# Kernel optimization log

Hardware: AMD Instinct MI355X
Metric: run time of the kernel (lower is better)

The kernel has to match this reference:

```python
import jax, jax.numpy as jnp
import numpy as np

NUM_EMBEDDINGS = 1024
EMBEDDING_DIM = 64
COMMITMENT_COST = 0.25


def setup_inputs() -> dict:
    key = jax.random.key(0)
    k1, k2 = jax.random.split(key)
    inputs = jax.random.normal(k1, (16, EMBEDDING_DIM, 64, 64), dtype=jnp.float32)
    # nn.Embedding weight init: uniform(-1/K, 1/K)
    emb = jax.random.uniform(
        k2, (NUM_EMBEDDINGS, EMBEDDING_DIM), dtype=jnp.float32,
        minval=-1.0 / NUM_EMBEDDINGS, maxval=1.0 / NUM_EMBEDDINGS)
    return {"inputs": inputs, "emb": emb}


def reference(inputs, emb):
    # NCHW -> NHWC
    x = jnp.transpose(inputs, (0, 2, 3, 1))  # [B,H,W,D]
    B, H, W, D = x.shape
    K = emb.shape[0]
    flat = x.reshape(-1, D)  # [N,D]

    # squared L2 distances to every codebook entry: [N,K]
    distances = (jnp.sum(flat * flat, axis=1, keepdims=True)
                 + jnp.sum(emb * emb, axis=1)
                 - 2.0 * jnp.matmul(flat, emb.T))
    idx = jnp.argmin(distances, axis=1)  # [N]
    indices = idx.reshape(B, H, W)[:, None]  # [B,1,H,W]

    # gather == one-hot @ emb, but without the dense matmul
    quantized = emb[idx].reshape(B, H, W, D)

    e_latent_loss = jnp.mean((jax.lax.stop_gradient(quantized) - x) ** 2)
    q_latent_loss = jnp.mean((quantized - jax.lax.stop_gradient(x)) ** 2)
    loss = q_latent_loss + COMMITMENT_COST * e_latent_loss

    # straight-through estimator
    quantized_st = x + jax.lax.stop_gradient(quantized - x)

    # one-hot encodings are part of the module's return contract
    encodings = jax.nn.one_hot(idx, K, dtype=jnp.float32)  # [N,K]
    avg_probs = jnp.mean(encodings, axis=0)
    perplexity = jnp.exp(-jnp.sum(avg_probs * jnp.log(avg_probs + 1e-10)))

    quantized_out = jnp.transpose(quantized_st, (0, 3, 1, 2))  # back to NCHW
    return (loss, quantized_out, perplexity, encodings, indices)
```

## Files before the change

kernel.cpp:

```cpp
#include <hip/hip_runtime.h>

#define NPIX    65536
#define D       64
#define KCODES  1024
#define PIXB    64
#define BLOCK   512
#define XPAD    68
#define CAP     64
#define GFAC    0.036f

#define QUANT_OFF 1
#define PERP_OFF  4194305
#define ENC_OFF   4194306u
#define IDX_OFF   71303170u

typedef float f32x4 __attribute__((ext_vector_type(4)));
typedef short bf16x8 __attribute__((ext_vector_type(8)));

__device__ __forceinline__ unsigned short f2bf(float f) {
    unsigned u = __float_as_uint(f);
    return (unsigned short)((u + 0x7fffu + ((u >> 16) & 1u)) >> 16);
}
__device__ __forceinline__ bf16x8 pack8(const float* p) {
    bf16x8 v;
    v[0] = (short)f2bf(p[0]); v[1] = (short)f2bf(p[1]);
    v[2] = (short)f2bf(p[2]); v[3] = (short)f2bf(p[3]);
    v[4] = (short)f2bf(p[4]); v[5] = (short)f2bf(p[5]);
    v[6] = (short)f2bf(p[6]); v[7] = (short)f2bf(p[7]);
    return v;
}

__global__ __launch_bounds__(256) void vq_init(const float* __restrict__ emb,
                                               double* __restrict__ loss_sum,
                                               int* __restrict__ counts,
                                               float* __restrict__ se) {
    int t = blockIdx.x * 256 + threadIdx.x;
    if (t == 0) *loss_sum = 0.0;
    if (t < KCODES) {
        counts[t] = 0;
        const float* e = emb + (size_t)t * D;
        float r[8];
        #pragma unroll
        for (int j = 0; j < 8; ++j) r[j] = __fmul_rn(e[j], e[j]);
        #pragma unroll
        for (int i = 8; i < D; i += 8)
            #pragma unroll
            for (int j = 0; j < 8; ++j)
                r[j] = __fadd_rn(r[j], __fmul_rn(e[i + j], e[i + j]));
        float X = __fadd_rn(__fadd_rn(r[0], r[1]), __fadd_rn(r[2], r[3]));
        float Y = __fadd_rn(__fadd_rn(r[4], r[5]), __fadd_rn(r[6], r[7]));
        se[t] = __fadd_rn(X, Y);
    }
}

__global__ __launch_bounds__(512) void vq_main(const float* __restrict__ in,
                                               const float* __restrict__ emb,
                                               const float* __restrict__ se,
                                               float* __restrict__ out,
                                               double* __restrict__ loss_sum,
                                               int* __restrict__ counts) {
    __shared__ float xs[PIXB][XPAD];
    __shared__ float sls[KCODES];
    __shared__ float wmin[8][PIXB];
    __shared__ float gate[PIXB];
    __shared__ float sxs[PIXB];
    __shared__ float smx[PIXB];
    __shared__ float semaxsq;
    __shared__ int   cnt[PIXB];
    __shared__ unsigned short list[PIXB][CAP];
    __shared__ int   skfin[PIXB];

    const int tid  = threadIdx.x;
    const int lane = tid & 63;
    const int wid  = tid >> 6;
    const int n0   = blockIdx.x * PIXB;
    const int b    = n0 >> 12;
    const int s0   = n0 & 4095;

    {
        const float* base = in + ((size_t)b << 18) + s0;
        #pragma unroll
        for (int i = 0; i < 8; ++i) {
            int d = wid + (i << 3);
            xs[lane][d] = base[((size_t)d << 12) + lane];
        }
        sls[tid] = se[tid];
        sls[tid + 512] = se[tid + 512];
    }
    __syncthreads();

    if (tid < PIXB) {
        float r[8];
        #pragma unroll
        for (int j = 0; j < 8; ++j) {
            float v = xs[tid][j];
            r[j] = __fmul_rn(v, v);
        }
        #pragma unroll
        for (int i = 8; i < D; i += 8)
            #pragma unroll
            for (int j = 0; j < 8; ++j) {
                float v = xs[tid][i + j];
                r[j] = __fadd_rn(r[j], __fmul_rn(v, v));
            }
        float X = __fadd_rn(__fadd_rn(r[0], r[1]), __fadd_rn(r[2], r[3]));
        float Y = __fadd_rn(__fadd_rn(r[4], r[5]), __fadd_rn(r[6], r[7]));
        sxs[tid] = __fadd_rn(X, Y);
        float mx = sls[tid << 4];
        #pragma unroll
        for (int j = 1; j < 16; ++j) mx = fmaxf(mx, sls[(tid << 4) + j]);
        smx[tid] = mx;
    }

    const int wbase = wid * 128;
    const int arow  = lane & 15;
    const int kgrp  = (lane >> 4) << 3;
    const int rbase = (lane >> 4) << 2;

    float mreg[4][4];
    #pragma unroll
    for (int pt = 0; pt < 4; ++pt)
        #pragma unroll
        for (int r = 0; r < 4; ++r) mreg[pt][r] = 3.0e38f;

    #pragma unroll
    for (int s = 0; s < 2; ++s) {
        const int cbase = wbase + s * 64;
        f32x4 acc[4][4];
        #pragma unroll
        for (int pt = 0; pt < 4; ++pt)
            #pragma unroll
            for (int kt = 0; kt < 4; ++kt) acc[pt][kt] = (f32x4){0.f, 0.f, 0.f, 0.f};
        #pragma unroll
        for (int ks = 0; ks < 2; ++ks) {
            bf16x8 af[4];
            #pragma unroll
            for (int pt = 0; pt < 4; ++pt)
                af[pt] = pack8(&xs[pt * 16 + arow][ks * 32 + kgrp]);
            #pragma unroll
            for (int kt = 0; kt < 4; ++kt) {
                int code = cbase + kt * 16 + arow;
                bf16x8 bf_ = pack8(emb + ((size_t)code << 6) + ks * 32 + kgrp);
                #pragma unroll
                for (int pt = 0; pt < 4; ++pt)
                    acc[pt][kt] = __builtin_amdgcn_mfma_f32_16x16x32_bf16(
                        af[pt], bf_, acc[pt][kt], 0, 0, 0);
            }
        }
        #pragma unroll
        for (int pt = 0; pt < 4; ++pt)
            #pragma unroll
            for (int kt = 0; kt < 4; ++kt) {
                int code = cbase + kt * 16 + arow;
                #pragma unroll
                for (int r = 0; r < 4; ++r) {
                    float sv = __fsub_rn(sls[code], __fmul_rn(2.0f, acc[pt][kt][r]));
                    mreg[pt][r] = fminf(mreg[pt][r], sv);
                }
            }
    }
    #pragma unroll
    for (int m = 1; m < 16; m <<= 1)
        #pragma unroll
        for (int pt = 0; pt < 4; ++pt)
            #pragma unroll
            for (int r = 0; r < 4; ++r)
                mreg[pt][r] = fminf(mreg[pt][r], __shfl_xor(mreg[pt][r], m));
    if (arow == 0) {
        #pragma unroll
        for (int pt = 0; pt < 4; ++pt)
            #pragma unroll
            for (int r = 0; r < 4; ++r)
                wmin[wid][pt * 16 + rbase + r] = mreg[pt][r];
    }
    __syncthreads();

    if (tid == 0) {
        float mx = smx[0];
        #pragma unroll
        for (int j = 1; j < PIXB; ++j) mx = fmaxf(mx, smx[j]);
        semaxsq = mx;
    }
    __syncthreads();

    if (tid < PIXB) {
        float gm = wmin[0][tid];
        #pragma unroll
        for (int w = 1; w < 8; ++w) gm = fminf(gm, wmin[w][tid]);
        gate[tid] = gm + GFAC * sqrtf(sxs[tid] * semaxsq);
        cnt[tid] = 0;
    }
    __syncthreads();

    #pragma unroll
    for (int s = 0; s < 2; ++s) {
        const int cbase = wbase + s * 64;
        f32x4 acc[4][4];
        #pragma unroll
        for (int pt = 0; pt < 4; ++pt)
            #pragma unroll
            for (int kt = 0; kt < 4; ++kt) acc[pt][kt] = (f32x4){0.f, 0.f, 0.f, 0.f};
        #pragma unroll
        for (int ks = 0; ks < 2; ++ks) {
            bf16x8 af[4];
            #pragma unroll
            for (int pt = 0; pt < 4; ++pt)
                af[pt] = pack8(&xs[pt * 16 + arow][ks * 32 + kgrp]);
            #pragma unroll
            for (int kt = 0; kt < 4; ++kt) {
                int code = cbase + kt * 16 + arow;
                bf16x8 bf_ = pack8(emb + ((size_t)code << 6) + ks * 32 + kgrp);
                #pragma unroll
                for (int pt = 0; pt < 4; ++pt)
                    acc[pt][kt] = __builtin_amdgcn_mfma_f32_16x16x32_bf16(
                        af[pt], bf_, acc[pt][kt], 0, 0, 0);
            }
        }
        #pragma unroll
        for (int pt = 0; pt < 4; ++pt)
            #pragma unroll
            for (int kt = 0; kt < 4; ++kt) {
                int code = cbase + kt * 16 + arow;
                #pragma unroll
                for (int r = 0; r < 4; ++r) {
                    float sv = __fsub_rn(sls[code], __fmul_rn(2.0f, acc[pt][kt][r]));
                    int px = pt * 16 + rbase + r;
                    if (sv <= gate[px]) {
                        int slot = atomicAdd(&cnt[px], 1);
                        if (slot < CAP) list[px][slot] = (unsigned short)code;
                    }
                }
            }
    }
    __syncthreads();

    {
        const int px = tid >> 3, c0 = tid & 7;
        const int cn = cnt[px];
        float bv = 3.0e38f;
        int   bk = 0x7fffffff;
        if (cn > CAP) {
            for (int k = c0; k < KCODES; k += 8) {
                const float* er = emb + ((size_t)k << 6);
                float m = 0.f;
                #pragma unroll
                for (int d = 0; d < D; ++d) m = fmaf(xs[px][d], er[d], m);
                float sv = __fsub_rn(__fadd_rn(sxs[px], sls[k]), __fmul_rn(2.0f, m));
                if (sv < bv || (sv == bv && k < bk)) { bv = sv; bk = k; }
            }
        } else {
            for (int i = c0; i < cn; i += 8) {
                int k = list[px][i];
                const float* er = emb + ((size_t)k << 6);
                float m = 0.f;
                #pragma unroll
                for (int d = 0; d < D; ++d) m = fmaf(xs[px][d], er[d], m);
                float sv = __fsub_rn(__fadd_rn(sxs[px], sls[k]), __fmul_rn(2.0f, m));
                if (sv < bv || (sv == bv && k < bk)) { bv = sv; bk = k; }
            }
        }
        #pragma unroll
        for (int m = 4; m; m >>= 1) {
            float ov = __shfl_xor(bv, m);
            int   ok = __shfl_xor(bk, m);
            if (ov < bv || (ov == bv && ok < bk)) { bv = ov; bk = ok; }
        }
        if (c0 == 0) {
            skfin[px] = bk;
            atomicAdd(&counts[bk], 1);
            out[IDX_OFF + (unsigned)(n0 + px)] = (float)bk;
        }
    }
    __syncthreads();

    if (tid < PIXB) {
        int bk2 = skfin[tid];
        const float* eq = emb + ((size_t)bk2 << 6);
        float* qout = out + QUANT_OFF + ((size_t)b << 18) + s0 + tid;
        float mse = 0.f;
        #pragma unroll
        for (int d = 0; d < D; ++d) {
            float q = eq[d];
            qout[(size_t)d << 12] = q;
            float df = q - xs[tid][d];
            mse = fmaf(df, df, mse);
        }
        #pragma unroll
        for (int off = 32; off; off >>= 1) mse += __shfl_down(mse, off);
        if (tid == 0) atomicAdd(loss_sum, (double)mse);
    }

    float4* dst4 = (float4*)(out + ENC_OFF + (size_t)n0 * KCODES + 2);
    for (int i = tid; i < 16383; i += BLOCK) {
        int flat = (i << 2) + 2;
        int r0 = flat >> 10;
        int r1 = (flat + 3) >> 10;
        int k0 = skfin[r0];
        int k1 = skfin[r1];
        int c  = flat & 1023;
        float4 v;
        v.x = (c == k0) ? 1.f : 0.f;
        v.y = (c + 1 == k0) ? 1.f : 0.f;
        v.z = (((flat + 2) & 1023) == k1) ? 1.f : 0.f;
        v.w = (((flat + 3) & 1023) == k1) ? 1.f : 0.f;
        dst4[i] = v;
    }
    if (tid == 0) {
        float2* dh = (float2*)(out + ENC_OFF + (size_t)n0 * KCODES);
        int kh = skfin[0];
        float2 h2; h2.x = (kh == 0) ? 1.f : 0.f; h2.y = (kh == 1) ? 1.f : 0.f;
        *dh = h2;
        float2* dt = (float2*)(out + ENC_OFF + (size_t)n0 * KCODES + 65534);
        int kt = skfin[63];
        float2 t2; t2.x = (kt == 1022) ? 1.f : 0.f; t2.y = (kt == 1023) ? 1.f : 0.f;
        *dt = t2;
    }
}

__global__ __launch_bounds__(256) void vq_fin(const double* __restrict__ loss_sum,
                                              const int* __restrict__ counts,
                                              float* __restrict__ out) {
    __shared__ double red[256];
    int t = threadIdx.x;
    double ent = 0.0;
    for (int k = t; k < KCODES; k += 256) {
        double p = (double)counts[k] / 65536.0;
        ent -= p * log(p + 1e-10);
    }
    red[t] = ent;
    __syncthreads();
    for (int o = 128; o; o >>= 1) {
        if (t < o) red[t] += red[t + o];
        __syncthreads();
    }
    if (t == 0) {
        out[PERP_OFF] = (float)exp(red[0]);
        out[0] = (float)(1.25 * (*loss_sum) / 4194304.0);
    }
}

extern "C" void kernel_launch(void* const* d_in, const int* in_sizes, int n_in,
                              void* d_out, int out_size, void* d_ws, size_t ws_size,
                              hipStream_t stream) {
    const float* in  = (const float*)d_in[0];
    const float* emb = (const float*)d_in[1];
    float* out = (float*)d_out;

    double* loss_sum = (double*)d_ws;
    int*    counts   = (int*)((char*)d_ws + 8);
    float*  se       = (float*)((char*)d_ws + 8 + 4096);

    vq_init<<<4, 256, 0, stream>>>(emb, loss_sum, counts, se);
    vq_main<<<NPIX / PIXB, BLOCK, 0, stream>>>(in, emb, se, out, loss_sum, counts);
    vq_fin<<<1, 256, 0, stream>>>(loss_sum, counts, out);
}
```

Measured before the change: 154.4 us.

## Precompute bf16 codebook and pixel tiles, hoist A fragments, parallelize quantized writeback

The init kernel now writes a bf16 copy of the codebook to workspace. The main kernel stores a bf16 copy of the pixel tile in shared memory, so MFMA operands come from single vector loads instead of per-element float-to-bf16 conversion in every pass. The A fragments are loaded once into registers and reused across both distance passes. The quantized-output and MSE writeback is spread across all 8 waves instead of one, at the cost of extra shared memory and registers, which may lower occupancy.

```diff
diff --git a/kernel.cpp b/kernel.cpp
--- a/kernel.cpp
+++ b/kernel.cpp
@@ -6,6 +6,7 @@
 #define PIXB    64
 #define BLOCK   512
 #define XPAD    68
+#define XBPAD   72
 #define CAP     64
 #define GFAC    0.036f
 
@@ -14,6 +15,7 @@
 #define ENC_OFF   4194306u
 #define IDX_OFF   71303170u
 
+
 typedef float f32x4 __attribute__((ext_vector_type(4)));
 typedef short bf16x8 __attribute__((ext_vector_type(8)));
 
@@ -21,19 +23,12 @@
     unsigned u = __float_as_uint(f);
     return (unsigned short)((u + 0x7fffu + ((u >> 16) & 1u)) >> 16);
 }
-__device__ __forceinline__ bf16x8 pack8(const float* p) {
-    bf16x8 v;
-    v[0] = (short)f2bf(p[0]); v[1] = (short)f2bf(p[1]);
-    v[2] = (short)f2bf(p[2]); v[3] = (short)f2bf(p[3]);
-    v[4] = (short)f2bf(p[4]); v[5] = (short)f2bf(p[5]);
-    v[6] = (short)f2bf(p[6]); v[7] = (short)f2bf(p[7]);
-    return v;
-}
 
 __global__ __launch_bounds__(256) void vq_init(const float* __restrict__ emb,
                                                double* __restrict__ loss_sum,
                                                int* __restrict__ counts,
-                                               float* __restrict__ se) {
+                                               float* __restrict__ se,
+                                               unsigned short* __restrict__ ebf) {
     int t = blockIdx.x * 256 + threadIdx.x;
     if (t == 0) *loss_sum = 0.0;
     if (t < KCODES) {
@@ -50,16 +45,20 @@
         float X = __fadd_rn(__fadd_rn(r[0], r[1]), __fadd_rn(r[2], r[3]));
         float Y = __fadd_rn(__fadd_rn(r[4], r[5]), __fadd_rn(r[6], r[7]));
         se[t] = __fadd_rn(X, Y);
+        #pragma unroll
+        for (int j = 0; j < D; ++j) ebf[(t << 6) + j] = f2bf(e[j]);
     }
 }
 
 __global__ __launch_bounds__(512) void vq_main(const float* __restrict__ in,
                                                const float* __restrict__ emb,
                                                const float* __restrict__ se,
+                                               const unsigned short* __restrict__ ebf,
                                                float* __restrict__ out,
                                                double* __restrict__ loss_sum,
                                                int* __restrict__ counts) {
     __shared__ float xs[PIXB][XPAD];
+    __shared__ unsigned short xb[PIXB][XBPAD];
     __shared__ float sls[KCODES];
     __shared__ float wmin[8][PIXB];
     __shared__ float gate[PIXB];
@@ -82,7 +81,9 @@
         #pragma unroll
         for (int i = 0; i < 8; ++i) {
             int d = wid + (i << 3);
-            xs[lane][d] = base[((size_t)d << 12) + lane];
+            float v = base[((size_t)d << 12) + lane];
+            xs[lane][d] = v;
+            xb[lane][d] = f2bf(v);
         }
         sls[tid] = se[tid];
         sls[tid + 512] = se[tid + 512];
@@ -117,6 +118,13 @@
     const int kgrp  = (lane >> 4) << 3;
     const int rbase = (lane >> 4) << 2;
 
+    bf16x8 af[2][4];
+    #pragma unroll
+    for (int ks = 0; ks < 2; ++ks)
+        #pragma unroll
+        for (int pt = 0; pt < 4; ++pt)
+            af[ks][pt] = *(const bf16x8*)&xb[pt * 16 + arow][ks * 32 + kgrp];
+
     float mreg[4][4];
     #pragma unroll
     for (int pt = 0; pt < 4; ++pt)
@@ -133,18 +141,14 @@
             for (int kt = 0; kt < 4; ++kt) acc[pt][kt] = (f32x4){0.f, 0.f, 0.f, 0.f};
         #pragma unroll
         for (int ks = 0; ks < 2; ++ks) {
-            bf16x8 af[4];
-            #pragma unroll
-            for (int pt = 0; pt < 4; ++pt)
-                af[pt] = pack8(&xs[pt * 16 + arow][ks * 32 + kgrp]);
             #pragma unroll
             for (int kt = 0; kt < 4; ++kt) {
                 int code = cbase + kt * 16 + arow;
-                bf16x8 bf_ = pack8(emb + ((size_t)code << 6) + ks * 32 + kgrp);
+                bf16x8 bf_ = *(const bf16x8*)(ebf + ((size_t)code << 6) + ks * 32 + kgrp);
                 #pragma unroll
                 for (int pt = 0; pt < 4; ++pt)
                     acc[pt][kt] = __builtin_amdgcn_mfma_f32_16x16x32_bf16(
-                        af[pt], bf_, acc[pt][kt], 0, 0, 0);
+                        af[ks][pt], bf_, acc[pt][kt], 0, 0, 0);
             }
         }
         #pragma unroll
@@ -202,18 +206,14 @@
             for (int kt = 0; kt < 4; ++kt) acc[pt][kt] = (f32x4){0.f, 0.f, 0.f, 0.f};
         #pragma unroll
         for (int ks = 0; ks < 2; ++ks) {
-            bf16x8 af[4];
-            #pragma unroll
-            for (int pt = 0; pt < 4; ++pt)
-                af[pt] = pack8(&xs[pt * 16 + arow][ks * 32 + kgrp]);
             #pragma unroll
             for (int kt = 0; kt < 4; ++kt) {
                 int code = cbase + kt * 16 + arow;
-                bf16x8 bf_ = pack8(emb + ((size_t)code << 6) + ks * 32 + kgrp);
+                bf16x8 bf_ = *(const bf16x8*)(ebf + ((size_t)code << 6) + ks * 32 + kgrp);
                 #pragma unroll
                 for (int pt = 0; pt < 4; ++pt)
                     acc[pt][kt] = __builtin_amdgcn_mfma_f32_16x16x32_bf16(
-                        af[pt], bf_, acc[pt][kt], 0, 0, 0);
+                        af[ks][pt], bf_, acc[pt][kt], 0, 0, 0);
             }
         }
         #pragma unroll
@@ -273,21 +273,20 @@
     }
     __syncthreads();
 
-    if (tid < PIXB) {
-        int bk2 = skfin[tid];
-        const float* eq = emb + ((size_t)bk2 << 6);
-        float* qout = out + QUANT_OFF + ((size_t)b << 18) + s0 + tid;
+    {
+        float* qbase = out + QUANT_OFF + ((size_t)b << 18) + s0;
         float mse = 0.f;
         #pragma unroll
-        for (int d = 0; d < D; ++d) {
-            float q = eq[d];
-            qout[(size_t)d << 12] = q;
-            float df = q - xs[tid][d];
+        for (int i = 0; i < 8; ++i) {
+            int d = (wid << 3) + i;
+            float q = emb[((size_t)skfin[lane] << 6) + d];
+            qbase[((size_t)d << 12) + lane] = q;
+            float df = q - xs[lane][d];
             mse = fmaf(df, df, mse);
         }
         #pragma unroll
         for (int off = 32; off; off >>= 1) mse += __shfl_down(mse, off);
-        if (tid == 0) atomicAdd(loss_sum, (double)mse);
+        if (lane == 0) atomicAdd(loss_sum, (double)mse);
     }
 
     float4* dst4 = (float4*)(out + ENC_OFF + (size_t)n0 * KCODES + 2);
@@ -346,11 +345,12 @@
     const float* emb = (const float*)d_in[1];
     float* out = (float*)d_out;
 
-    double* loss_sum = (double*)d_ws;
-    int*    counts   = (int*)((char*)d_ws + 8);
-    float*  se       = (float*)((char*)d_ws + 8 + 4096);
-
-    vq_init<<<4, 256, 0, stream>>>(emb, loss_sum, counts, se);
-    vq_main<<<NPIX / PIXB, BLOCK, 0, stream>>>(in, emb, se, out, loss_sum, counts);
+    double*         loss_sum = (double*)d_ws;
+    int*            counts   = (int*)((char*)d_ws + 8);
+    float*          se       = (float*)((char*)d_ws + 4104);
+    unsigned short* ebf      = (unsigned short*)((char*)d_ws + 8320);
+
+    vq_init<<<4, 256, 0, stream>>>(emb, loss_sum, counts, se, ebf);
+    vq_main<<<NPIX / PIXB, BLOCK, 0, stream>>>(in, emb, se, ebf, out, loss_sum, counts);
     vq_fin<<<1, 256, 0, stream>>>(loss_sum, counts, out);
 }
```

Result: slower. 185.5 us (+20.1%).
